# Kernel tuning notes

Measured on AMD Instinct MI355X. Metric: run time of the kernel, lower is better.

## Reference

```python
import jax, jax.numpy as jnp
import numpy as np

V, L, H, D, T, B = 32000, 8, 16, 1024, 1024, 2
HD = D // H
SCALE = 1.0 / float(np.sqrt(HD))


def setup_inputs() -> dict:
    key = jax.random.key(0)
    ks = jax.random.split(key, 8)
    s = 0.02
    def n(k, shape):
        return jax.random.normal(k, shape, jnp.float32) * s
    return {
        "input_ids": jax.random.randint(ks[0], (B, T), 0, V),
        "tok_emb": n(ks[1], (V, D)),            # tied with lm_head
        "pos_emb": n(ks[2], (T, D)),
        "ln1_w": jnp.ones((L, D)), "ln1_b": jnp.zeros((L, D)),
        "qkv_w": n(ks[3], (L, D, 3 * D)),       # no bias in qkv_proj
        "out_w": n(ks[4], (L, D, D)), "out_b": jnp.zeros((L, D)),
        "ln2_w": jnp.ones((L, D)), "ln2_b": jnp.zeros((L, D)),
        "fc1_w": n(ks[5], (L, D, 4 * D)), "fc1_b": jnp.zeros((L, 4 * D)),
        "fc2_w": n(ks[6], (L, 4 * D, D)), "fc2_b": jnp.zeros((L, D)),
        "lnf_w": jnp.ones((D,)), "lnf_b": jnp.zeros((D,)),
    }


def _ln(x, w, b):
    m = x.mean(-1, keepdims=True)
    v = x.var(-1, keepdims=True)
    return (x - m) * jax.lax.rsqrt(v + 1e-5) * w + b


def _gpt(input_ids, tok_emb, pos_emb, ln1_w, ln1_b, qkv_w, out_w, out_b,
         ln2_w, ln2_b, fc1_w, fc1_b, fc2_w, fc2_b, lnf_w, lnf_b):
    Bq, Tq = input_ids.shape
    x = tok_emb[input_ids] + pos_emb[:Tq][None]          # [B,T,D]
    causal = jnp.tril(jnp.ones((Tq, Tq), bool))          # [T,T]

    def layer(x, p):
        l1w, l1b, qw, ow, ob, l2w, l2b, f1w, f1b, f2w, f2b = p
        h = _ln(x, l1w, l1b)
        qkv = h @ qw                                     # [B,T,3D]
        q, k, v = jnp.split(qkv, 3, axis=-1)
        q = q.reshape(Bq, Tq, H, HD)
        k = k.reshape(Bq, Tq, H, HD)
        v = v.reshape(Bq, Tq, H, HD)
        att = jnp.einsum('bqhd,bkhd->bhqk', q, k) * SCALE
        att = jnp.where(causal, att, -jnp.inf)
        att = jax.nn.softmax(att, axis=-1)
        o = jnp.einsum('bhqk,bkhd->bqhd', att, v).reshape(Bq, Tq, D)
        x = x + o @ ow + ob
        h2 = _ln(x, l2w, l2b)
        x = x + jax.nn.gelu(h2 @ f1w + f1b, approximate=False) @ f2w + f2b
        return x, None

    x, _ = jax.lax.scan(layer, x, (ln1_w, ln1_b, qkv_w, out_w, out_b,
                                   ln2_w, ln2_b, fc1_w, fc1_b, fc2_w, fc2_b))
    x = _ln(x, lnf_w, lnf_b)
    return x @ tok_emb.T                                 # tied lm_head


def reference(input_ids, tok_emb, pos_emb, ln1_w, ln1_b, qkv_w, out_w, out_b,
              ln2_w, ln2_b, fc1_w, fc1_b, fc2_w, fc2_b, lnf_w, lnf_b):
    return _gpt(input_ids, tok_emb, pos_emb, ln1_w, ln1_b, qkv_w, out_w, out_b,
                ln2_w, ln2_b, fc1_w, fc1_b, fc2_w, fc2_b, lnf_w, lnf_b)
```

## Files before the change

kernel.cpp:

```cpp
#include <hip/hip_runtime.h>
#include <hip/hip_bf16.h>
#include <math.h>


#define DEV_INLINE __device__ __forceinline__

typedef float  f32x4  __attribute__((ext_vector_type(4)));
typedef __bf16 bf16x8 __attribute__((ext_vector_type(8)));
typedef short  s16x4  __attribute__((ext_vector_type(4)));
typedef short  s16x8  __attribute__((ext_vector_type(8)));
typedef unsigned int u32x4 __attribute__((ext_vector_type(4)));

#define BBATCH 2
#define TSEQ   1024
#define DMODEL 1024
#define NHEAD  16
#define HDIM   64
#define NLAYER 8
#define NVOCAB 32000
#define MTOK   (BBATCH*TSEQ)

DEV_INLINE short f2bf(float f) {
    __bf16 h = (__bf16)f;
    union { __bf16 h; short s; } u; u.h = h; return u.s;
}

typedef const __attribute__((address_space(1))) unsigned int* gas_t;
typedef __attribute__((address_space(3))) unsigned int* las_t;
DEV_INLINE void llds16(const void* g, void* l) {
    __builtin_amdgcn_global_load_lds((gas_t)g, (las_t)l, 16, 0, 0);
}

#define BAR()  asm volatile("s_barrier" ::: "memory")
#define VMW4() asm volatile("s_waitcnt vmcnt(4)" ::: "memory")
#define VMW2() asm volatile("s_waitcnt vmcnt(2)" ::: "memory")
#define VMW0() asm volatile("s_waitcnt vmcnt(0)" ::: "memory")

DEV_INLINE float block_sum(float v) {
    __shared__ float sb[4];
    #pragma unroll
    for (int o = 32; o > 0; o >>= 1) v += __shfl_down(v, o, 64);
    if ((threadIdx.x & 63) == 0) sb[threadIdx.x >> 6] = v;
    __syncthreads();
    float r = sb[0] + sb[1] + sb[2] + sb[3];
    __syncthreads();
    return r;
}

__global__ __launch_bounds__(256) void flash_k(
    const short* __restrict__ qkv, const short* __restrict__ Vt,
    short* __restrict__ O)
{
    const int qb = blockIdx.x;
    const int z  = blockIdx.y;
    const int zb = z >> 4, zh = z & 15;

    __shared__ short Qs[128 * 64];
    __shared__ short KP[128 * 136];
    __shared__ short Vs[64 * 128];

    const int tid  = threadIdx.x;
    const int w    = tid >> 6, lane = tid & 63;
    const int lr   = lane & 15, kg = lane >> 4;

    const long long qbase = (long long)zb * TSEQ * 3072;
    const short* Qg = qkv + qbase + zh * HDIM;
    const short* Kg = qkv + qbase + DMODEL + zh * HDIM;
    const short* Vg = Vt + (long long)z * (HDIM * TSEQ);

    const int sr   = tid >> 3, pc = tid & 7;
    const int lc   = pc ^ (sr & 7);
    const int sr16 = tid >> 4, pc16 = tid & 15;

    {
        const short* qp = Qg + (long long)(qb * 128 + sr) * 3072 + lc * 8;
        const short* kp = Kg + (long long)(0 + sr) * 3072 + lc * 8;
        #pragma unroll
        for (int it = 0; it < 4; ++it) {
            llds16(qp + (long long)it * 32 * 3072, Qs + tid * 8 + it * 2048);
            llds16(kp + (long long)it * 32 * 3072, KP + tid * 8 + it * 2048);
        }
        #pragma unroll
        for (int it = 0; it < 4; ++it) {
            const int r = it * 16 + sr16;
            const int lc2 = pc16 ^ (r & 7);
            llds16(Vg + (long long)r * TSEQ + 0 + lc2 * 8, Vs + tid * 8 + it * 2048);
        }
    }
    __syncthreads();
    bf16x8 afq[2][2];
    #pragma unroll
    for (int s = 0; s < 2; ++s)
        #pragma unroll
        for (int i = 0; i < 2; ++i) {
            const int r = w * 32 + i * 16 + lr;
            afq[s][i] = *(const bf16x8*)&Qs[r * 64 + (((s * 4 + kg) ^ (r & 7)) << 3)];
        }

    f32x4 aco[2][4] = {};
    float m_[2][4], l_[2][4];
    #pragma unroll
    for (int i = 0; i < 2; ++i)
        #pragma unroll
        for (int p = 0; p < 4; ++p) { m_[i][p] = -1e30f; l_[i][p] = 0.f; }

    const int nt = qb + 1;
    for (int t = 0; t < nt; ++t) {
        u32x4 kpre[4], vpre[4];
        const bool nx = (t + 1 < nt);
        if (nx) {
            const int kn = (t + 1) * 128;
            #pragma unroll
            for (int it = 0; it < 4; ++it)
                kpre[it] = *(const u32x4*)(Kg + (long long)(kn + sr + it * 32) * 3072 + lc * 8);
            #pragma unroll
            for (int it = 0; it < 4; ++it) {
                const int r = it * 16 + sr16;
                const int lc2 = pc16 ^ (r & 7);
                vpre[it] = *(const u32x4*)(Vg + (long long)r * TSEQ + kn + lc2 * 8);
            }
            __builtin_amdgcn_sched_barrier(0);
        }

        f32x4 acs[2][8] = {};
        #pragma unroll
        for (int s = 0; s < 2; ++s)
            #pragma unroll
            for (int j = 0; j < 8; ++j) {
                const int rk = j * 16 + lr;
                bf16x8 bk = *(const bf16x8*)&KP[rk * 64 + (((s * 4 + kg) ^ (rk & 7)) << 3)];
                #pragma unroll
                for (int i = 0; i < 2; ++i)
                    acs[i][j] = __builtin_amdgcn_mfma_f32_16x16x32_bf16(
                        afq[s][i], bk, acs[i][j], 0, 0, 0);
            }

        #pragma unroll
        for (int i = 0; i < 2; ++i)
            #pragma unroll
            for (int j = 0; j < 8; ++j)
                #pragma unroll
                for (int p = 0; p < 4; ++p) {
                    float v = acs[i][j][p] * 0.125f;
                    if (t == qb && (j * 16 + lr) > (w * 32 + i * 16 + kg * 4 + p))
                        v = -1e30f;
                    acs[i][j][p] = v;
                }

        float sc[2][4];
        #pragma unroll
        for (int i = 0; i < 2; ++i)
            #pragma unroll
            for (int p = 0; p < 4; ++p) {
                float r = acs[i][0][p];
                #pragma unroll
                for (int j = 1; j < 8; ++j) r = fmaxf(r, acs[i][j][p]);
                r = fmaxf(r, __shfl_xor(r, 1, 64));
                r = fmaxf(r, __shfl_xor(r, 2, 64));
                r = fmaxf(r, __shfl_xor(r, 4, 64));
                r = fmaxf(r, __shfl_xor(r, 8, 64));
                const float mn = fmaxf(m_[i][p], r);
                sc[i][p] = __expf(m_[i][p] - mn);
                m_[i][p] = mn;
            }
        #pragma unroll
        for (int i = 0; i < 2; ++i)
            #pragma unroll
            for (int j = 0; j < 8; ++j)
                #pragma unroll
                for (int p = 0; p < 4; ++p)
                    acs[i][j][p] = __expf(acs[i][j][p] - m_[i][p]);
        #pragma unroll
        for (int i = 0; i < 2; ++i)
            #pragma unroll
            for (int p = 0; p < 4; ++p) {
                float s = 0.f;
                #pragma unroll
                for (int j = 0; j < 8; ++j) s += acs[i][j][p];
                s += __shfl_xor(s, 1, 64);
                s += __shfl_xor(s, 2, 64);
                s += __shfl_xor(s, 4, 64);
                s += __shfl_xor(s, 8, 64);
                l_[i][p] = l_[i][p] * sc[i][p] + s;
            }
        #pragma unroll
        for (int i = 0; i < 2; ++i)
            #pragma unroll
            for (int j2 = 0; j2 < 4; ++j2)
                #pragma unroll
                for (int p = 0; p < 4; ++p)
                    aco[i][j2][p] *= sc[i][p];

        __syncthreads();

        #pragma unroll
        for (int i = 0; i < 2; ++i)
            #pragma unroll
            for (int j = 0; j < 8; ++j)
                #pragma unroll
                for (int p = 0; p < 4; ++p)
                    KP[(w * 32 + i * 16 + kg * 4 + p) * 136 + j * 16 + lr] =
                        f2bf(acs[i][j][p]);
        __syncthreads();

        #pragma unroll
        for (int ks = 0; ks < 4; ++ks) {
            bf16x8 pa[2], pb[4];
            #pragma unroll
            for (int i = 0; i < 2; ++i)
                pa[i] = *(const bf16x8*)&KP[(w * 32 + i * 16 + lr) * 136 + ks * 32 + kg * 8];
            #pragma unroll
            for (int j2 = 0; j2 < 4; ++j2) {
                const int d = j2 * 16 + lr;
                pb[j2] = *(const bf16x8*)&Vs[d * 128 + (((ks * 4 + kg) ^ (d & 7)) << 3)];
            }
            #pragma unroll
            for (int i = 0; i < 2; ++i)
                #pragma unroll
                for (int j2 = 0; j2 < 4; ++j2)
                    aco[i][j2] = __builtin_amdgcn_mfma_f32_16x16x32_bf16(
                        pa[i], pb[j2], aco[i][j2], 0, 0, 0);
        }
        __syncthreads();

        if (nx) {
            #pragma unroll
            for (int it = 0; it < 4; ++it)
                *(u32x4*)(KP + tid * 8 + it * 2048) = kpre[it];
            #pragma unroll
            for (int it = 0; it < 4; ++it)
                *(u32x4*)(Vs + tid * 8 + it * 2048) = vpre[it];
            __syncthreads();
        }
    }

    #pragma unroll
    for (int i = 0; i < 2; ++i)
        #pragma unroll
        for (int j2 = 0; j2 < 4; ++j2)
            #pragma unroll
            for (int p = 0; p < 4; ++p) {
                const int row = zb * TSEQ + qb * 128 + w * 32 + i * 16 + kg * 4 + p;
                const int col = zh * HDIM + j2 * 16 + lr;
                O[(long long)row * DMODEL + col] = f2bf(aco[i][j2][p] / l_[i][p]);
            }
}

__global__ __launch_bounds__(512, 2) void gemm256_k(
    const short* __restrict__ A, const short* __restrict__ B,
    float* __restrict__ C, int K, int lda, int ldb, int ldc, int gx)
{
    extern __shared__ short smem[];

    const int nwg = gridDim.x;
    int wg = blockIdx.x;
    int sw = (wg & 7) * (nwg >> 3) + (wg >> 3);
    const int bx = sw >> 3, by = sw & 7;
    const int bn0 = bx * 256, bm0 = by * 256;

    const int tid  = threadIdx.x;
    const int w    = tid >> 6, lane = tid & 63;
    const int wm   = w >> 2, wn = w & 3;
    const int lr   = lane & 15, kg = lane >> 4;

    const int r0  = tid >> 3;
    const int pc  = tid & 7;
    const int lc0 = pc ^ (r0 & 7);
    const int r1  = r0 + 64;
    const int lc1 = pc ^ (r1 & 7);

    f32x4 acc[2][2][4][2] = {};
    const int nk = K >> 6;

    auto stage = [&](int buf, int isA, int h, int kk) {
        const short* gp = isA ? A : B;
        const int    ld = isA ? lda : ldb;
        const long long rb = (long long)((isA ? bm0 : bn0) + h * 128);
        short* lp = smem + buf * 32768 + (isA ? 0 : 16384) + h * 8192;
        llds16(gp + (rb + r0) * ld + kk + lc0 * 8, lp + w * 512);
        llds16(gp + (rb + r1) * ld + kk + lc1 * 8, lp + 4096 + w * 512);
    };

#define PHASE(BUF, QM, QN, ISA, H, DOWAIT)                                      \
    do {                                                                        \
        const short* Ah = smem + (BUF) * 32768 + (QM) * 8192;                   \
        const short* Bh = smem + (BUF) * 32768 + 16384 + (QN) * 8192;           \
        bf16x8 af[2][4], bfr[2][2];                                             \
        _Pragma("unroll")                                                       \
        for (int s2 = 0; s2 < 2; ++s2) {                                        \
            _Pragma("unroll")                                                   \
            for (int i = 0; i < 4; ++i) {                                       \
                const int ra = wm * 64 + i * 16 + lr;                           \
                af[s2][i] = *(const bf16x8*)                                    \
                    &Ah[ra * 64 + (((s2 * 4 + kg) ^ (ra & 7)) << 3)];           \
            }                                                                   \
            _Pragma("unroll")                                                   \
            for (int j = 0; j < 2; ++j) {                                       \
                const int rb2 = wn * 32 + j * 16 + lr;                          \
                bfr[s2][j] = *(const bf16x8*)                                   \
                    &Bh[rb2 * 64 + (((s2 * 4 + kg) ^ (rb2 & 7)) << 3)];         \
            }                                                                   \
        }                                                                       \
        if (pf) stage(nb, ISA, H, kk);                                          \
        BAR();                                                                  \
        __builtin_amdgcn_s_setprio(1);                                          \
        _Pragma("unroll")                                                       \
        for (int s2 = 0; s2 < 2; ++s2)                                          \
            _Pragma("unroll")                                                   \
            for (int i = 0; i < 4; ++i)                                         \
                _Pragma("unroll")                                               \
                for (int j = 0; j < 2; ++j)                                     \
                    acc[QM][QN][i][j] = __builtin_amdgcn_mfma_f32_16x16x32_bf16(\
                        af[s2][i], bfr[s2][j], acc[QM][QN][i][j], 0, 0, 0);     \
        __builtin_amdgcn_s_setprio(0);                                          \
        DOWAIT;                                                                 \
        BAR();                                                                  \
    } while (0)

    stage(0, 1, 0, 0);
    stage(0, 0, 0, 0);
    stage(0, 1, 1, 0);
    stage(0, 0, 1, 0);
    if (nk > 1) { VMW4(); } else { VMW0(); }
    BAR();

    for (int t = 0; t < nk - 1; ++t) {
        const int  buf = t & 1, nb = buf ^ 1;
        const int  kk  = (t + 1) << 6;
        const bool pf  = true;
        PHASE(buf, 0, 0, 1, 0, VMW4());
        PHASE(buf, 1, 0, 0, 0, VMW4());
        PHASE(buf, 1, 1, 1, 1, (void)0);
        PHASE(buf, 0, 1, 0, 1, VMW4());
    }
    {
        const int  buf = (nk - 1) & 1, nb = buf ^ 1; (void)nb;
        const int  kk  = 0;
        const bool pf  = false;
        PHASE(buf, 0, 0, 1, 0, VMW2());
        PHASE(buf, 1, 0, 0, 0, VMW0());
        PHASE(buf, 1, 1, 1, 1, (void)0);
        PHASE(buf, 0, 1, 0, 1, (void)0);
    }
#undef PHASE

    #pragma unroll
    for (int qm = 0; qm < 2; ++qm)
        #pragma unroll
        for (int qn = 0; qn < 2; ++qn)
            #pragma unroll
            for (int i = 0; i < 4; ++i)
                #pragma unroll
                for (int j = 0; j < 2; ++j) {
                    const int gr = bm0 + qm * 128 + wm * 64 + i * 16 + kg * 4;
                    const int gc = bn0 + qn * 128 + wn * 32 + j * 16 + lr;
                    #pragma unroll
                    for (int p = 0; p < 4; ++p)
                        C[(long long)(gr + p) * ldc + gc] = acc[qm][qn][i][j][p];
                }
}

template<int BN, int EPI>
__global__ __launch_bounds__(256) void gemm_k(
    const short* __restrict__ Ag, const short* __restrict__ Bg,
    void* __restrict__ Cg, const float* __restrict__ bias,
    short* __restrict__ aux,
    int M, int N, int K, int lda, int ldb, int ldc,
    long long sAz, long long sBz, long long sCz,
    float scale, int swz)
{
    int bx = blockIdx.x, by = blockIdx.y;
    if (swz) {
        const int gx = gridDim.x;
        const int nwg = gx * gridDim.y;
        if ((nwg & 7) == 0) {
            int wg = by * gx + bx;
            int wg2 = (wg & 7) * (nwg >> 3) + (wg >> 3);
            bx = wg2 % gx; by = wg2 / gx;
        }
    }
    const int bn0 = bx * BN, bm0 = by * 128;
    const int zz = blockIdx.z;

    const short* A = Ag + zz * sAz;
    const short* B = Bg + zz * sBz;

    __shared__ short Als[2][128 * 64];
    __shared__ short Bls[2][BN * 64];

    const int tid  = threadIdx.x;
    const int lane = tid & 63;
    const int wave = tid >> 6;
    constexpr int WMS = (BN == 128) ? 64 : 32;
    constexpr int MI  = (BN == 128) ? 4 : 2;
    constexpr int NJ  = 4;
    const int wm = (BN == 128) ? (wave >> 1) : wave;
    const int wn = (BN == 128) ? (wave & 1) : 0;
    const int lr = lane & 15, kg = lane >> 4;
    const int xv = (lr & 7) << 4;

    const int sr = tid >> 3;
    const int sc = (tid & 7) ^ (sr & 7);
    const short* aP = A + (long long)(bm0 + sr) * lda + sc * 8;
    const short* bP = B + (long long)(bn0 + sr) * ldb + sc * 8;

    f32x4 acc[MI][NJ] = {};
    const int nk = K >> 6;

    auto stage = [&](int buf, int kt) {
        const int k0 = kt << 6;
        short* aL = &Als[buf][wave * 512];
        short* bL = &Bls[buf][wave * 512];
        #pragma unroll
        for (int it = 0; it < 4; ++it)
            llds16(aP + (long long)it * 32 * lda + k0, aL + it * 2048);
        #pragma unroll
        for (int it = 0; it < BN / 32; ++it)
            llds16(bP + (long long)it * 32 * ldb + k0, bL + it * 2048);
    };

    stage(0, 0);
    __syncthreads();

    for (int kt = 0; kt < nk; ++kt) {
        const int cb = kt & 1;
        if (kt + 1 < nk) stage(cb ^ 1, kt + 1);

        #pragma unroll
        for (int s = 0; s < 2; ++s) {
            const int ofs = (((s << 6) | (kg << 4)) ^ xv) >> 1;
            bf16x8 af[MI], bf[NJ];
            #pragma unroll
            for (int i = 0; i < MI; ++i)
                af[i] = *(const bf16x8*)&Als[cb][(wm * WMS + i * 16 + lr) * 64 + ofs];
            #pragma unroll
            for (int j = 0; j < NJ; ++j)
                bf[j] = *(const bf16x8*)&Bls[cb][(wn * 64 + j * 16 + lr) * 64 + ofs];
            #pragma unroll
            for (int i = 0; i < MI; ++i)
                #pragma unroll
                for (int j = 0; j < NJ; ++j)
                    acc[i][j] = __builtin_amdgcn_mfma_f32_16x16x32_bf16(
                        af[i], bf[j], acc[i][j], 0, 0, 0);
        }
        __syncthreads();
    }

    short* Cs = (short*)Cg + zz * sCz;
    float* Cf = (float*)Cg + zz * sCz;
    #pragma unroll
    for (int i = 0; i < MI; ++i) {
        #pragma unroll
        for (int j = 0; j < NJ; ++j) {
            const int gr = bm0 + wm * WMS + i * 16 + kg * 4;
            const int gc = bn0 + wn * 64 + j * 16 + lr;
            if (EPI == 4 && gc >= 2 * DMODEL) {
                const int b = gr >> 10, t0 = gr & (TSEQ - 1);
                const int h = (gc - 2 * DMODEL) >> 6, d = gc & 63;
                s16x4 vv;
                #pragma unroll
                for (int p = 0; p < 4; ++p) vv[p] = f2bf(acc[i][j][p]);
                *(s16x4*)&aux[((long long)(b * NHEAD + h) * HDIM + d) * TSEQ + t0] = vv;
            } else {
                #pragma unroll
                for (int p = 0; p < 4; ++p) {
                    const long long off = (long long)(gr + p) * ldc + gc;
                    float v = acc[i][j][p];
                    if (EPI == 0) {
                        Cf[off] = v;
                    } else if (EPI == 1 || EPI == 4) {
                        Cs[off] = f2bf(v * scale);
                    } else {
                        v += bias[gc];
                        v = 0.5f * v * (1.0f + erff(v * 0.70710678118654752f));
                        Cs[off] = f2bf(v);
                    }
                }
            }
        }
    }
}

template<int NP>
__global__ __launch_bounds__(256) void fredln_k(
    const float* __restrict__ fp, long long pstride,
    const float* __restrict__ bias, float* __restrict__ x,
    const float* __restrict__ lw, const float* __restrict__ lb,
    short* __restrict__ o)
{
    const int row  = blockIdx.x * 4 + (threadIdx.x >> 6);
    const int lane = threadIdx.x & 63;
    const long long base = (long long)row * DMODEL + lane * 16;
    const int cb = lane * 16;
    float4 v[4];
    #pragma unroll
    for (int q = 0; q < 4; ++q) {
        v[q] = *(const float4*)&x[base + q * 4];
        float4 bb = *(const float4*)&bias[cb + q * 4];
        v[q].x += bb.x; v[q].y += bb.y; v[q].z += bb.z; v[q].w += bb.w;
        #pragma unroll
        for (int k = 0; k < NP; ++k) {
            float4 pp = *(const float4*)&fp[k * pstride + base + q * 4];
            v[q].x += pp.x; v[q].y += pp.y; v[q].z += pp.z; v[q].w += pp.w;
        }
        *(float4*)&x[base + q * 4] = v[q];
    }
    float s = 0.f, s2 = 0.f;
    #pragma unroll
    for (int q = 0; q < 4; ++q) {
        s  += v[q].x + v[q].y + v[q].z + v[q].w;
        s2 += v[q].x * v[q].x + v[q].y * v[q].y + v[q].z * v[q].z + v[q].w * v[q].w;
    }
    #pragma unroll
    for (int d = 1; d < 64; d <<= 1) {
        s  += __shfl_xor(s, d, 64);
        s2 += __shfl_xor(s2, d, 64);
    }
    const float mean = s * (1.0f / DMODEL);
    const float var  = s2 * (1.0f / DMODEL) - mean * mean;
    const float rs   = rsqrtf(var + 1e-5f);
    short ov[16];
    #pragma unroll
    for (int q = 0; q < 4; ++q) {
        float4 wv = *(const float4*)&lw[cb + q * 4];
        float4 bv = *(const float4*)&lb[cb + q * 4];
        ov[q * 4 + 0] = f2bf((v[q].x - mean) * rs * wv.x + bv.x);
        ov[q * 4 + 1] = f2bf((v[q].y - mean) * rs * wv.y + bv.y);
        ov[q * 4 + 2] = f2bf((v[q].z - mean) * rs * wv.z + bv.z);
        ov[q * 4 + 3] = f2bf((v[q].w - mean) * rs * wv.w + bv.w);
    }
    short* op = o + base;
    *(s16x8*)op       = *(s16x8*)&ov[0];
    *(s16x8*)(op + 8) = *(s16x8*)&ov[8];
}

__global__ __launch_bounds__(256) void embedln_k(
    const int* __restrict__ ids, const float* __restrict__ tok,
    const float* __restrict__ pos, float* __restrict__ x,
    const float* __restrict__ lw, const float* __restrict__ lb,
    short* __restrict__ o)
{
    const int row = blockIdx.x;
    const int t   = row & (TSEQ - 1);
    const int id  = ids[row];
    const int i   = threadIdx.x * 4;
    const long long base = (long long)row * DMODEL;
    float4 a = *(const float4*)&tok[(long long)id * DMODEL + i];
    float4 p = *(const float4*)&pos[(long long)t * DMODEL + i];
    float4 v;
    v.x = a.x + p.x; v.y = a.y + p.y; v.z = a.z + p.z; v.w = a.w + p.w;
    *(float4*)&x[base + i] = v;
    float s  = v.x + v.y + v.z + v.w;
    float s2 = v.x * v.x + v.y * v.y + v.z * v.z + v.w * v.w;
    s  = block_sum(s);
    s2 = block_sum(s2);
    const float mean = s * (1.0f / DMODEL);
    const float var  = s2 * (1.0f / DMODEL) - mean * mean;
    const float rs   = rsqrtf(var + 1e-5f);
    float4 wv = *(const float4*)&lw[i];
    float4 bv = *(const float4*)&lb[i];
    s16x4 ov;
    ov[0] = f2bf((v.x - mean) * rs * wv.x + bv.x);
    ov[1] = f2bf((v.y - mean) * rs * wv.y + bv.y);
    ov[2] = f2bf((v.z - mean) * rs * wv.z + bv.z);
    ov[3] = f2bf((v.w - mean) * rs * wv.w + bv.w);
    *(s16x4*)&o[base + i] = ov;
}

template<typename T>
DEV_INLINE void tcvt_body(const T* sp, short* dp, int lds_, int ldd,
                          int bx, int by, short (*ls)[68], int t)
{
    const int tr0 = by * 64, tc0 = bx * 64;
    const int rr = t >> 4, cc = (t & 15) * 4;
    #pragma unroll
    for (int q = 0; q < 4; ++q) {
        const int r = q * 16 + rr;
        if constexpr (sizeof(T) == 4) {
            float4 v = *(const float4*)&sp[(long long)(tr0 + r) * lds_ + tc0 + cc];
            ls[cc + 0][r] = f2bf(v.x); ls[cc + 1][r] = f2bf(v.y);
            ls[cc + 2][r] = f2bf(v.z); ls[cc + 3][r] = f2bf(v.w);
        } else {
            s16x4 v = *(const s16x4*)&sp[(long long)(tr0 + r) * lds_ + tc0 + cc];
            ls[cc + 0][r] = v[0]; ls[cc + 1][r] = v[1];
            ls[cc + 2][r] = v[2]; ls[cc + 3][r] = v[3];
        }
    }
    __syncthreads();
    #pragma unroll
    for (int q = 0; q < 4; ++q) {
        const int c = q * 16 + rr;
        s16x4 v;
        v[0] = ls[c][cc]; v[1] = ls[c][cc + 1]; v[2] = ls[c][cc + 2]; v[3] = ls[c][cc + 3];
        *(s16x4*)&dp[(long long)(tc0 + c) * ldd + tr0 + cc] = v;
    }
}

template<typename T>
__global__ __launch_bounds__(256) void tcvt_k(
    const T* __restrict__ src, short* __restrict__ dst,
    int lds_, int ldd, int Hdiv,
    long long sSb, long long sSh, long long sDb, long long sDh)
{
    __shared__ short ls[64][68];
    const int z = blockIdx.z, zb = z / Hdiv, zh = z - zb * Hdiv;
    tcvt_body<T>(src + zb * sSb + zh * sSh, dst + zb * sDb + zh * sDh,
                 lds_, ldd, blockIdx.x, blockIdx.y, ls, threadIdx.x);
}

__global__ __launch_bounds__(256) void wcvt_k(
    const float* __restrict__ qw, const float* __restrict__ ow,
    const float* __restrict__ f1, const float* __restrict__ f2,
    short* __restrict__ wq, short* __restrict__ wo,
    short* __restrict__ w1, short* __restrict__ w2)
{
    __shared__ short ls[64][68];
    const int id = blockIdx.x;
    const float* src; short* dst; int lds_, ldd, bx, by;
    if (id < 768)       { src = qw; dst = wq; lds_ = 3072; ldd = 1024; bx = id % 48;  by = id / 48; }
    else if (id < 1024) { int i = id - 768;  src = ow; dst = wo; lds_ = 1024; ldd = 1024; bx = i % 16; by = i / 16; }
    else if (id < 2048) { int i = id - 1024; src = f1; dst = w1; lds_ = 4096; ldd = 1024; bx = i % 64; by = i / 64; }
    else                { int i = id - 2048; src = f2; dst = w2; lds_ = 1024; ldd = 4096; bx = i % 16; by = i / 16; }
    tcvt_body<float>(src, dst, lds_, ldd, bx, by, ls, threadIdx.x);
}

__global__ __launch_bounds__(256) void cvt_k(
    const float* __restrict__ s, short* __restrict__ d, int n4)
{
    int i = blockIdx.x * 256 + threadIdx.x;
    const int stride = gridDim.x * 256;
    for (; i < n4; i += stride) {
        float4 v = *(const float4*)&s[(long long)i * 4];
        s16x4 o = { f2bf(v.x), f2bf(v.y), f2bf(v.z), f2bf(v.w) };
        *(s16x4*)&d[(long long)i * 4] = o;
    }
}

extern "C" void kernel_launch(void* const* d_in, const int* in_sizes, int n_in,
                              void* d_out, int out_size, void* d_ws, size_t ws_size,
                              hipStream_t stream)
{
    const int*   ids  = (const int*)  d_in[0];
    const float* tok  = (const float*)d_in[1];
    const float* pos  = (const float*)d_in[2];
    const float* ln1w = (const float*)d_in[3];
    const float* ln1b = (const float*)d_in[4];
    const float* qkvw = (const float*)d_in[5];
    const float* outw = (const float*)d_in[6];
    const float* outb = (const float*)d_in[7];
    const float* ln2w = (const float*)d_in[8];
    const float* ln2b = (const float*)d_in[9];
    const float* fc1w = (const float*)d_in[10];
    const float* fc1b = (const float*)d_in[11];
    const float* fc2w = (const float*)d_in[12];
    const float* fc2b = (const float*)d_in[13];
    const float* lnfw = (const float*)d_in[14];
    const float* lnfb = (const float*)d_in[15];
    float* out = (float*)d_out;

    char* ws = (char*)d_ws;
    const size_t MB = 1024 * 1024;
    float* x    = (float*)(ws);
    short* hb   = (short*)(ws + 8  * MB);
    short* qkvb = (short*)(ws + 12 * MB);
    short* g    = (short*)(ws + 24 * MB);
    short* Vt   = (short*)(ws + 40 * MB);
    float* fp   = (float*)(ws + 44 * MB);
    short* tokb = (short*)(ws + 12 * MB);

    const bool big = ws_size >= (size_t)272 * MB;
    short* wq = (short*)(ws + 80 * MB);
    short *wo, *w1, *w2;
    if (big) {
        wo = (short*)(ws + 128 * MB);
        w1 = (short*)(ws + 144 * MB);
        w2 = (short*)(ws + 208 * MB);
    } else {
        wo = (short*)(ws + 86 * MB);
        w1 = (short*)(ws + 88 * MB);
        w2 = (short*)(ws + 96 * MB);
    }

    const long long LWQ = 3072LL * 1024, LWO = 1024LL * 1024;
    const long long LW1 = 4096LL * 1024, LW2 = 1024LL * 4096;
    const long long MD  = (long long)MTOK * DMODEL;

    hipFuncSetAttribute((const void*)gemm256_k,
                        hipFuncAttributeMaxDynamicSharedMemorySize, 131072);

    dim3 blk(256);
    embedln_k<<<MTOK, blk, 0, stream>>>(ids, tok, pos, x, ln1w, ln1b, hb);

    if (big) {
        tcvt_k<float><<<dim3(48, 16, 8), blk, 0, stream>>>(qkvw, wq, 3072, 1024, 1, LWQ, 0, LWQ, 0);
        tcvt_k<float><<<dim3(16, 16, 8), blk, 0, stream>>>(outw, wo, 1024, 1024, 1, LWO, 0, LWO, 0);
        tcvt_k<float><<<dim3(64, 16, 8), blk, 0, stream>>>(fc1w, w1, 4096, 1024, 1, LW1, 0, LW1, 0);
        tcvt_k<float><<<dim3(16, 64, 8), blk, 0, stream>>>(fc2w, w2, 1024, 4096, 1, LW2, 0, LW2, 0);
    }

    for (int l = 0; l < NLAYER; ++l) {
        short* wql = wq + (big ? l * LWQ : 0);
        short* wol = wo + (big ? l * LWO : 0);
        short* w1l = w1 + (big ? l * LW1 : 0);
        short* w2l = w2 + (big ? l * LW2 : 0);
        if (!big)
            wcvt_k<<<3072, blk, 0, stream>>>(
                qkvw + l * LWQ, outw + l * LWO, fc1w + l * LW1, fc2w + l * LW2,
                wql, wol, w1l, w2l);

        gemm_k<128, 4><<<dim3(24, 16, 1), blk, 0, stream>>>(
            hb, wql, qkvb, nullptr, Vt,
            MTOK, 3 * DMODEL, DMODEL, DMODEL, DMODEL, 3 * DMODEL,
            0, 0, 0, 1.0f, 1);

        flash_k<<<dim3(8, BBATCH * NHEAD), blk, 0, stream>>>(qkvb, Vt, hb);

        gemm_k<128, 0><<<dim3(8, 16, 2), blk, 0, stream>>>(
            hb, wol, fp, nullptr, nullptr,
            MTOK, DMODEL, 512, DMODEL, DMODEL, DMODEL,
            512, 512, MD, 1.0f, 1);
        fredln_k<2><<<MTOK / 4, blk, 0, stream>>>(
            fp, MD, outb + l * DMODEL, x,
            ln2w + l * DMODEL, ln2b + l * DMODEL, hb);

        gemm_k<128, 3><<<dim3(32, 16, 1), blk, 0, stream>>>(
            hb, w1l, g, fc1b + (long long)l * 4 * DMODEL, nullptr,
            MTOK, 4 * DMODEL, DMODEL, DMODEL, DMODEL, 4 * DMODEL,
            0, 0, 0, 1.0f, 1);

        gemm_k<128, 0><<<dim3(8, 16, 4), blk, 0, stream>>>(
            g, w2l, fp, nullptr, nullptr,
            MTOK, DMODEL, 1024, 4 * DMODEL, 4 * DMODEL, DMODEL,
            1024, 1024, MD, 1.0f, 1);
        const float* nlw = (l < 7) ? ln1w + (l + 1) * DMODEL : lnfw;
        const float* nlb = (l < 7) ? ln1b + (l + 1) * DMODEL : lnfb;
        fredln_k<4><<<MTOK / 4, blk, 0, stream>>>(
            fp, MD, fc2b + l * DMODEL, x, nlw, nlb, hb);
    }

    cvt_k<<<2048, blk, 0, stream>>>(tok, tokb, NVOCAB * DMODEL / 4);

    gemm256_k<<<dim3((NVOCAB / 256) * (MTOK / 256)), dim3(512), 131072, stream>>>(
        hb, tokb, out, DMODEL, DMODEL, DMODEL, NVOCAB, NVOCAB / 256);
}
```

Baseline: 1.585 ms.

## Split long causal flash-attention query blocks across two workgroups and merge partials

The heavy query blocks (qb 4-7) of the causal attention are split into two KV-range halves handled by separate workgroups. Each half writes fp32 partial outputs plus row max and sum to workspace, and a new merge kernel combines them with log-sum-exp rescaling. This balances the triangular workload and raises the grid from 256 to 384 workgroups, at the cost of an extra launch and fp32 partial traffic. Separately, the GEMM tile swizzle gains a column-major remap mode (swz=2), now used by all per-layer GEMMs to change the L2 reuse pattern.

```diff
diff --git a/kernel.cpp b/kernel.cpp
--- a/kernel.cpp
+++ b/kernel.cpp
@@ -49,11 +49,20 @@
 
 __global__ __launch_bounds__(256) void flash_k(
     const short* __restrict__ qkv, const short* __restrict__ Vt,
-    short* __restrict__ O)
-{
-    const int qb = blockIdx.x;
+    short* __restrict__ O, float* __restrict__ Op, float* __restrict__ ml)
+{
+    const int bxi = blockIdx.x;
     const int z  = blockIdx.y;
     const int zb = z >> 4, zh = z & 15;
+
+    int qb, t0, t1, ph; bool part;
+    if (bxi < 8) {
+        qb = 4 + (bxi >> 1); ph = bxi & 1;
+        const int nt = qb + 1, h0 = (nt + 1) >> 1;
+        t0 = ph ? h0 : 0; t1 = ph ? nt : h0; part = true;
+    } else {
+        qb = bxi - 8; t0 = 0; t1 = qb + 1; ph = 0; part = false;
+    }
 
     __shared__ short Qs[128 * 64];
     __shared__ short KP[128 * 136];
@@ -73,8 +82,9 @@
     const int sr16 = tid >> 4, pc16 = tid & 15;
 
     {
+        const int kv0 = t0 * 128;
         const short* qp = Qg + (long long)(qb * 128 + sr) * 3072 + lc * 8;
-        const short* kp = Kg + (long long)(0 + sr) * 3072 + lc * 8;
+        const short* kp = Kg + (long long)(kv0 + sr) * 3072 + lc * 8;
         #pragma unroll
         for (int it = 0; it < 4; ++it) {
             llds16(qp + (long long)it * 32 * 3072, Qs + tid * 8 + it * 2048);
@@ -84,7 +94,7 @@
         for (int it = 0; it < 4; ++it) {
             const int r = it * 16 + sr16;
             const int lc2 = pc16 ^ (r & 7);
-            llds16(Vg + (long long)r * TSEQ + 0 + lc2 * 8, Vs + tid * 8 + it * 2048);
+            llds16(Vg + (long long)r * TSEQ + kv0 + lc2 * 8, Vs + tid * 8 + it * 2048);
         }
     }
     __syncthreads();
@@ -104,10 +114,9 @@
         #pragma unroll
         for (int p = 0; p < 4; ++p) { m_[i][p] = -1e30f; l_[i][p] = 0.f; }
 
-    const int nt = qb + 1;
-    for (int t = 0; t < nt; ++t) {
+    for (int t = t0; t < t1; ++t) {
         u32x4 kpre[4], vpre[4];
-        const bool nx = (t + 1 < nt);
+        const bool nx = (t + 1 < t1);
         if (nx) {
             const int kn = (t + 1) * 128;
             #pragma unroll
@@ -234,16 +243,74 @@
         }
     }
 
-    #pragma unroll
-    for (int i = 0; i < 2; ++i)
-        #pragma unroll
-        for (int j2 = 0; j2 < 4; ++j2)
-            #pragma unroll
-            for (int p = 0; p < 4; ++p) {
-                const int row = zb * TSEQ + qb * 128 + w * 32 + i * 16 + kg * 4 + p;
-                const int col = zh * HDIM + j2 * 16 + lr;
-                O[(long long)row * DMODEL + col] = f2bf(aco[i][j2][p] / l_[i][p]);
-            }
+    if (!part) {
+        #pragma unroll
+        for (int i = 0; i < 2; ++i)
+            #pragma unroll
+            for (int j2 = 0; j2 < 4; ++j2)
+                #pragma unroll
+                for (int p = 0; p < 4; ++p) {
+                    const int row = zb * TSEQ + qb * 128 + w * 32 + i * 16 + kg * 4 + p;
+                    const int col = zh * HDIM + j2 * 16 + lr;
+                    O[(long long)row * DMODEL + col] = f2bf(aco[i][j2][p] / l_[i][p]);
+                }
+    } else {
+        const long long pb = ((long long)z * 4 + (qb - 4)) * 2 + ph;
+        float* op  = Op + pb * (128 * 64);
+        float* mlp = ml + pb * (128 * 2);
+        #pragma unroll
+        for (int i = 0; i < 2; ++i)
+            #pragma unroll
+            for (int j2 = 0; j2 < 4; ++j2)
+                #pragma unroll
+                for (int p = 0; p < 4; ++p)
+                    op[(w * 32 + i * 16 + kg * 4 + p) * 64 + j2 * 16 + lr] = aco[i][j2][p];
+        if (lr == 0) {
+            #pragma unroll
+            for (int i = 0; i < 2; ++i)
+                #pragma unroll
+                for (int p = 0; p < 4; ++p) {
+                    const int r = w * 32 + i * 16 + kg * 4 + p;
+                    mlp[r * 2]     = m_[i][p];
+                    mlp[r * 2 + 1] = l_[i][p];
+                }
+        }
+    }
+}
+
+__global__ __launch_bounds__(256) void merge_k(
+    const float* __restrict__ Op, const float* __restrict__ ml,
+    short* __restrict__ O)
+{
+    const int b = blockIdx.x;
+    const int z = b >> 2, qb4 = b & 3;
+    const int zb = z >> 4, zh = z & 15;
+    const float* o0  = Op + ((long long)b * 2 + 0) * (128 * 64);
+    const float* o1  = Op + ((long long)b * 2 + 1) * (128 * 64);
+    const float* ml0 = ml + ((long long)b * 2 + 0) * 256;
+    const float* ml1 = ml + ((long long)b * 2 + 1) * 256;
+
+    const int r  = threadIdx.x >> 1;
+    const int c0 = (threadIdx.x & 1) * 32;
+    const float m0 = ml0[r * 2], l0 = ml0[r * 2 + 1];
+    const float m1 = ml1[r * 2], l1 = ml1[r * 2 + 1];
+    const float M  = fmaxf(m0, m1);
+    const float w0 = __expf(m0 - M), w1 = __expf(m1 - M);
+    const float inv = 1.0f / (w0 * l0 + w1 * l1);
+
+    const int grow = zb * TSEQ + (qb4 + 4) * 128 + r;
+    short* dst = O + (long long)grow * DMODEL + zh * HDIM + c0;
+    #pragma unroll
+    for (int cc = 0; cc < 32; cc += 4) {
+        float4 a = *(const float4*)&o0[r * 64 + c0 + cc];
+        float4 bq = *(const float4*)&o1[r * 64 + c0 + cc];
+        s16x4 ov;
+        ov[0] = f2bf((w0 * a.x + w1 * bq.x) * inv);
+        ov[1] = f2bf((w0 * a.y + w1 * bq.y) * inv);
+        ov[2] = f2bf((w0 * a.z + w1 * bq.z) * inv);
+        ov[3] = f2bf((w0 * a.w + w1 * bq.w) * inv);
+        *(s16x4*)&dst[cc] = ov;
+    }
 }
 
 __global__ __launch_bounds__(512, 2) void gemm256_k(
@@ -371,12 +438,13 @@
 {
     int bx = blockIdx.x, by = blockIdx.y;
     if (swz) {
-        const int gx = gridDim.x;
-        const int nwg = gx * gridDim.y;
+        const int gx = gridDim.x, gy = gridDim.y;
+        const int nwg = gx * gy;
         if ((nwg & 7) == 0) {
             int wg = by * gx + bx;
             int wg2 = (wg & 7) * (nwg >> 3) + (wg >> 3);
-            bx = wg2 % gx; by = wg2 / gx;
+            if (swz == 2) { bx = wg2 / gy; by = wg2 - bx * gy; }
+            else          { bx = wg2 % gx; by = wg2 / gx; }
         }
     }
     const int bn0 = bx * BN, bm0 = by * 128;
@@ -666,6 +734,8 @@
     short* g    = (short*)(ws + 24 * MB);
     short* Vt   = (short*)(ws + 40 * MB);
     float* fp   = (float*)(ws + 44 * MB);
+    float* Opb  = (float*)(ws + 44 * MB);
+    float* mlb  = (float*)(ws + 61 * MB);
     short* tokb = (short*)(ws + 12 * MB);
 
     const bool big = ws_size >= (size_t)272 * MB;
@@ -711,14 +781,16 @@
         gemm_k<128, 4><<<dim3(24, 16, 1), blk, 0, stream>>>(
             hb, wql, qkvb, nullptr, Vt,
             MTOK, 3 * DMODEL, DMODEL, DMODEL, DMODEL, 3 * DMODEL,
-            0, 0, 0, 1.0f, 1);
-
-        flash_k<<<dim3(8, BBATCH * NHEAD), blk, 0, stream>>>(qkvb, Vt, hb);
+            0, 0, 0, 1.0f, 2);
+
+        flash_k<<<dim3(12, BBATCH * NHEAD), blk, 0, stream>>>(
+            qkvb, Vt, hb, Opb, mlb);
+        merge_k<<<128, blk, 0, stream>>>(Opb, mlb, hb);
 
         gemm_k<128, 0><<<dim3(8, 16, 2), blk, 0, stream>>>(
             hb, wol, fp, nullptr, nullptr,
             MTOK, DMODEL, 512, DMODEL, DMODEL, DMODEL,
-            512, 512, MD, 1.0f, 1);
+            512, 512, MD, 1.0f, 2);
         fredln_k<2><<<MTOK / 4, blk, 0, stream>>>(
             fp, MD, outb + l * DMODEL, x,
             ln2w + l * DMODEL, ln2b + l * DMODEL, hb);
@@ -726,12 +798,12 @@
         gemm_k<128, 3><<<dim3(32, 16, 1), blk, 0, stream>>>(
             hb, w1l, g, fc1b + (long long)l * 4 * DMODEL, nullptr,
             MTOK, 4 * DMODEL, DMODEL, DMODEL, DMODEL, 4 * DMODEL,
-            0, 0, 0, 1.0f, 1);
+            0, 0, 0, 1.0f, 2);
 
         gemm_k<128, 0><<<dim3(8, 16, 4), blk, 0, stream>>>(
             g, w2l, fp, nullptr, nullptr,
             MTOK, DMODEL, 1024, 4 * DMODEL, 4 * DMODEL, DMODEL,
-            1024, 1024, MD, 1.0f, 1);
+            1024, 1024, MD, 1.0f, 2);
         const float* nlw = (l < 7) ? ln1w + (l + 1) * DMODEL : lnfw;
         const float* nlb = (l < 7) ? ln1b + (l + 1) * DMODEL : lnfb;
         fredln_k<4><<<MTOK / 4, blk, 0, stream>>>(
```

After: 1.709 ms. 7.8% more time.
